# Performance work log

Hardware: AMD Instinct MI355X
Metric: run time of the kernel (lower is better)

## Reference

```python
import jax, jax.numpy as jnp
import numpy as np

N_PIX = 65536   # 256x256 render
N_GAUSS = 2048
N_COL = 3


def setup_inputs() -> dict:
    key = jax.random.key(0)
    k1, k2, k3, k4 = jax.random.split(key, 4)
    x = jax.random.uniform(k1, (N_PIX, 2), dtype=jnp.float32)           # pixel coords
    mus = jax.random.uniform(k2, (N_GAUSS, 2), dtype=jnp.float32)       # Gaussian means
    # SPD covariances: A A^T + sigma*I  (small spatial extent ~0.05)
    A = jax.random.normal(k3, (N_GAUSS, 2, 2), dtype=jnp.float32) * 0.05
    covs = jnp.einsum('mij,mkj->mik', A, A) + 0.01 * jnp.eye(2, dtype=jnp.float32)
    cols = jax.random.uniform(k4, (N_GAUSS, N_COL), dtype=jnp.float32)  # RGB per Gaussian
    return {"x": x, "mus": mus, "covs": covs, "cols": cols}


def reference(x, mus, covs, cols):
    # d: [N, M, 2] pixel-to-mean offsets
    d = x[:, None, :] - mus[None, :, :]
    # solve(covs, d) per (pixel, Gaussian) == cov_inv @ d; covs depend only on Gaussian,
    # so invert once per Gaussian (same math as torch.linalg.solve per pair).
    cov_inv = jnp.linalg.inv(covs)                      # [M, 2, 2]
    maha = jnp.einsum('nmi,mij,nmj->nm', d, cov_inv, d)  # [N, M] Mahalanobis distances
    w = jnp.exp(-0.5 * maha)                             # [N, M] Gaussian weights
    # weighted sum of colors over Gaussians: [N, M] @ [M, 3] -> [N, 3]
    return jnp.einsum('nm,mc->nc', w, cols)
```

## Files before the change

kernel.cpp:

```cpp
#include <hip/hip_runtime.h>

#define N_PIX   65536
#define N_GAUSS 2048

typedef __bf16 bf16x8 __attribute__((ext_vector_type(8)));
typedef float  f32x4  __attribute__((ext_vector_type(4)));

union BF8U { uint4 u; bf16x8 h; };
__device__ inline bf16x8 as_bf(uint4 u) { BF8U x; x.u = u; return x.h; }

__device__ inline unsigned short bfbits(float f) {
  __bf16 h = (__bf16)f;
  return __builtin_bit_cast(unsigned short, h);
}
__device__ inline float bf2f(unsigned short b) {
  return (float)__builtin_bit_cast(__bf16, b);
}
__device__ inline unsigned pkb(unsigned short a, unsigned short b) {
  return (unsigned)a | ((unsigned)b << 16);
}
__device__ inline unsigned pk2f(float a, float b) {
  return pkb(bfbits(a), bfbits(b));
}


__global__ __launch_bounds__(256) void prep_kernel(
    const float* __restrict__ mus, const float* __restrict__ covs,
    const float* __restrict__ cols, uint4* __restrict__ ws) {
  int tid = blockIdx.x * 256 + threadIdx.x;
  if (tid < 8192) {
    int lane = tid & 63;
    int tile = tid >> 6;
    int grp  = lane >> 4;
    int g    = tile * 16 + (lane & 15);
    float c00 = covs[4*g+0], c01 = covs[4*g+1];
    float c10 = covs[4*g+2], c11 = covs[4*g+3];
    float inv_det = 1.0f / (c00*c11 - c01*c10);
    float ia =  c11 * inv_det;
    float ib = -c01 * inv_det;
    float ic =  c00 * inv_det;
    float mx = mus[2*g+0], my = mus[2*g+1];
    const float kk = -0.7213475204444817f;
    float coef[6];
    coef[0] = kk * ia;
    coef[1] = kk * 2.0f * ib;
    coef[2] = kk * ic;
    coef[3] = -2.0f * kk * (ia*mx + ib*my);
    coef[4] = -2.0f * kk * (ib*mx + ic*my);
    coef[5] = kk * (ia*mx*mx + 2.0f*ib*mx*my + ic*my*my);
    unsigned short ch[6], cl[6];
    #pragma unroll
    for (int i = 0; i < 6; ++i) {
      ch[i] = bfbits(coef[i]);
      cl[i] = bfbits(coef[i] - bf2f(ch[i]));
    }
    uint4 v = make_uint4(0,0,0,0);
    if (grp == 0)      v = make_uint4(pkb(ch[0],ch[1]), pkb(ch[2],ch[3]), pkb(ch[4],ch[5]), pkb(cl[0],cl[1]));
    else if (grp == 1) v = make_uint4(pkb(cl[2],cl[3]), pkb(cl[4],cl[5]), pkb(ch[0],ch[1]), pkb(ch[2],ch[3]));
    else if (grp == 2) v = make_uint4(pkb(ch[4],ch[5]), pkb(cl[0],cl[1]), pkb(cl[2],cl[3]), pkb(cl[4],cl[5]));
    ws[tid] = v;
  } else if (tid < 12288) {
    int t2   = tid - 8192;
    int lane = t2 & 63;
    int tile = t2 >> 6;
    int rgb  = lane & 15;
    int kb   = (lane >> 4) * 8;
    uint4 v = make_uint4(0,0,0,0);
    if (rgb < 3) {
      unsigned short b[8];
      #pragma unroll
      for (int j = 0; j < 8; ++j)
        b[j] = bfbits(cols[(tile*32 + kb + j)*3 + rgb]);
      v = make_uint4(pkb(b[0],b[1]), pkb(b[2],b[3]), pkb(b[4],b[5]), pkb(b[6],b[7]));
    }
    ws[8192 + t2] = v;
  }
}

__global__ __launch_bounds__(512, 4) void render_kernel(
    const float2* __restrict__ x, const uint4* __restrict__ ws,
    float* __restrict__ out) {
  __shared__ uint4 smem[1536];
  const uint4* gq  = ws;
  const uint4* pvc = ws + 8192;

  int tid  = threadIdx.x;
  int lane = tid & 63, wave = tid >> 6;
  int c    = lane & 15, grp = lane >> 4;
  int wpix = blockIdx.x * 128 + wave * 16;

  float2 p = x[wpix + c];
  float mono[6] = {p.x*p.x, p.x*p.y, p.y*p.y, p.x, p.y, 1.0f};
  unsigned short ph[6], pl[6];
  #pragma unroll
  for (int i = 0; i < 6; ++i) {
    ph[i] = bfbits(mono[i]);
    pl[i] = bfbits(mono[i] - bf2f(ph[i]));
  }
  uint4 pv4 = make_uint4(0,0,0,0);
  if (grp == 0)      pv4 = make_uint4(pkb(ph[0],ph[1]), pkb(ph[2],ph[3]), pkb(ph[4],ph[5]), pkb(ph[0],ph[1]));
  else if (grp == 1) pv4 = make_uint4(pkb(ph[2],ph[3]), pkb(ph[4],ph[5]), pkb(pl[0],pl[1]), pkb(pl[2],pl[3]));
  else if (grp == 2) pv4 = make_uint4(pkb(pl[4],pl[5]), pkb(pl[0],pl[1]), pkb(pl[2],pl[3]), pkb(pl[4],pl[5]));
  bf16x8 pf = as_bf(pv4);

  char* Wb = (char*)smem + 16384 + (wave << 10);
  int b0 = c*64 + grp*8;
  int b1 = c*64 + 32 + grp*8;
  int br = c*64 + grp*16;
  uint2* wp0 = (uint2*)(Wb + (b0 ^ (((b0 >> 7) & 3) << 4)));
  uint2* wp1 = (uint2*)(Wb + (b1 ^ (((b1 >> 7) & 3) << 4)));
  const uint4* rp = (const uint4*)(Wb + (br ^ (((br >> 7) & 3) << 4)));

  f32x4 acc  = {0.f, 0.f, 0.f, 0.f};
  const f32x4 zero = {0.f, 0.f, 0.f, 0.f};

  uint4 s0 = gq[tid], s1 = gq[512 + tid];
  for (int chk = 0; chk < 8; ++chk) {
    __syncthreads();
    smem[tid] = s0; smem[512 + tid] = s1;
    __syncthreads();
    if (chk < 7) {
      s0 = gq[(chk+1)*1024 + tid];
      s1 = gq[(chk+1)*1024 + 512 + tid];
    }
    uint4 cf[8];
    #pragma unroll
    for (int t = 0; t < 8; ++t)
      cf[t] = pvc[chk*512 + t*64 + lane];
    #pragma unroll
    for (int pr = 0; pr < 8; ++pr) {
      uint4 ga = smem[(2*pr+0)*64 + lane];
      uint4 gb = smem[(2*pr+1)*64 + lane];
      f32x4 q0 = __builtin_amdgcn_mfma_f32_16x16x32_bf16(as_bf(ga), pf, zero, 0, 0, 0);
      f32x4 q1 = __builtin_amdgcn_mfma_f32_16x16x32_bf16(as_bf(gb), pf, zero, 0, 0, 0);
      uint2 w0, w1;
      w0.x = pk2f(__builtin_amdgcn_exp2f(q0[0]), __builtin_amdgcn_exp2f(q0[1]));
      w0.y = pk2f(__builtin_amdgcn_exp2f(q0[2]), __builtin_amdgcn_exp2f(q0[3]));
      w1.x = pk2f(__builtin_amdgcn_exp2f(q1[0]), __builtin_amdgcn_exp2f(q1[1]));
      w1.y = pk2f(__builtin_amdgcn_exp2f(q1[2]), __builtin_amdgcn_exp2f(q1[3]));
      *wp0 = w0;
      *wp1 = w1;
      asm volatile("s_waitcnt lgkmcnt(0)" ::: "memory");
      uint4 wf = *rp;
      acc = __builtin_amdgcn_mfma_f32_16x16x32_bf16(as_bf(wf), as_bf(cf[pr]), acc, 0, 0, 0);
    }
  }
  if (c < 3) {
    int pix = wpix + grp * 4;
    out[(pix+0)*3 + c] = acc[0];
    out[(pix+1)*3 + c] = acc[1];
    out[(pix+2)*3 + c] = acc[2];
    out[(pix+3)*3 + c] = acc[3];
  }
}

extern "C" void kernel_launch(void* const* d_in, const int* in_sizes, int n_in,
                              void* d_out, int out_size, void* d_ws, size_t ws_size,
                              hipStream_t stream) {
  const float* x    = (const float*)d_in[0];
  const float* mus  = (const float*)d_in[1];
  const float* covs = (const float*)d_in[2];
  const float* cols = (const float*)d_in[3];
  float* out = (float*)d_out;
  uint4* ws  = (uint4*)d_ws;

  prep_kernel<<<48, 256, 0, stream>>>(mus, covs, cols, ws);
  render_kernel<<<512, 512, 0, stream>>>((const float2*)x, ws, out);
}
```

Before: 84.87 us.

## Feed exp weights directly as MFMA operand, removing LDS transpose round-trip

Swaps the operand roles in the second MFMA so the packed exp2 results held in registers can serve directly as the B operand. The prep kernel reorders the color-tile K indices to match the register layout of the first MFMA's output. This removes a per-iteration LDS write, waitcnt and read, and shrinks shared memory. The output store now writes three channels per pixel from one lane group.

```diff
diff --git a/kernel.cpp b/kernel.cpp
--- a/kernel.cpp
+++ b/kernel.cpp
@@ -64,13 +64,15 @@
     int lane = t2 & 63;
     int tile = t2 >> 6;
     int rgb  = lane & 15;
-    int kb   = (lane >> 4) * 8;
+    int grp  = lane >> 4;
     uint4 v = make_uint4(0,0,0,0);
     if (rgb < 3) {
       unsigned short b[8];
       #pragma unroll
-      for (int j = 0; j < 8; ++j)
-        b[j] = bfbits(cols[(tile*32 + kb + j)*3 + rgb]);
+      for (int j = 0; j < 8; ++j) {
+        int sig = 4*grp + (j & 3) + ((j >> 2) ? 16 : 0);
+        b[j] = bfbits(cols[(tile*32 + sig)*3 + rgb]);
+      }
       v = make_uint4(pkb(b[0],b[1]), pkb(b[2],b[3]), pkb(b[4],b[5]), pkb(b[6],b[7]));
     }
     ws[8192 + t2] = v;
@@ -80,13 +82,14 @@
 __global__ __launch_bounds__(512, 4) void render_kernel(
     const float2* __restrict__ x, const uint4* __restrict__ ws,
     float* __restrict__ out) {
-  __shared__ uint4 smem[1536];
+  __shared__ uint4 smem[1024];
   const uint4* gq  = ws;
   const uint4* pvc = ws + 8192;
 
   int tid  = threadIdx.x;
-  int lane = tid & 63, wave = tid >> 6;
+  int lane = tid & 63;
   int c    = lane & 15, grp = lane >> 4;
+  int wave = tid >> 6;
   int wpix = blockIdx.x * 128 + wave * 16;
 
   float2 p = x[wpix + c];
@@ -102,14 +105,6 @@
   else if (grp == 1) pv4 = make_uint4(pkb(ph[2],ph[3]), pkb(ph[4],ph[5]), pkb(pl[0],pl[1]), pkb(pl[2],pl[3]));
   else if (grp == 2) pv4 = make_uint4(pkb(pl[4],pl[5]), pkb(pl[0],pl[1]), pkb(pl[2],pl[3]), pkb(pl[4],pl[5]));
   bf16x8 pf = as_bf(pv4);
-
-  char* Wb = (char*)smem + 16384 + (wave << 10);
-  int b0 = c*64 + grp*8;
-  int b1 = c*64 + 32 + grp*8;
-  int br = c*64 + grp*16;
-  uint2* wp0 = (uint2*)(Wb + (b0 ^ (((b0 >> 7) & 3) << 4)));
-  uint2* wp1 = (uint2*)(Wb + (b1 ^ (((b1 >> 7) & 3) << 4)));
-  const uint4* rp = (const uint4*)(Wb + (br ^ (((br >> 7) & 3) << 4)));
 
   f32x4 acc  = {0.f, 0.f, 0.f, 0.f};
   const f32x4 zero = {0.f, 0.f, 0.f, 0.f};
@@ -133,24 +128,19 @@
       uint4 gb = smem[(2*pr+1)*64 + lane];
       f32x4 q0 = __builtin_amdgcn_mfma_f32_16x16x32_bf16(as_bf(ga), pf, zero, 0, 0, 0);
       f32x4 q1 = __builtin_amdgcn_mfma_f32_16x16x32_bf16(as_bf(gb), pf, zero, 0, 0, 0);
-      uint2 w0, w1;
-      w0.x = pk2f(__builtin_amdgcn_exp2f(q0[0]), __builtin_amdgcn_exp2f(q0[1]));
-      w0.y = pk2f(__builtin_amdgcn_exp2f(q0[2]), __builtin_amdgcn_exp2f(q0[3]));
-      w1.x = pk2f(__builtin_amdgcn_exp2f(q1[0]), __builtin_amdgcn_exp2f(q1[1]));
-      w1.y = pk2f(__builtin_amdgcn_exp2f(q1[2]), __builtin_amdgcn_exp2f(q1[3]));
-      *wp0 = w0;
-      *wp1 = w1;
-      asm volatile("s_waitcnt lgkmcnt(0)" ::: "memory");
-      uint4 wf = *rp;
-      acc = __builtin_amdgcn_mfma_f32_16x16x32_bf16(as_bf(wf), as_bf(cf[pr]), acc, 0, 0, 0);
+      unsigned w0 = pk2f(__builtin_amdgcn_exp2f(q0[0]), __builtin_amdgcn_exp2f(q0[1]));
+      unsigned w1 = pk2f(__builtin_amdgcn_exp2f(q0[2]), __builtin_amdgcn_exp2f(q0[3]));
+      unsigned w2 = pk2f(__builtin_amdgcn_exp2f(q1[0]), __builtin_amdgcn_exp2f(q1[1]));
+      unsigned w3 = pk2f(__builtin_amdgcn_exp2f(q1[2]), __builtin_amdgcn_exp2f(q1[3]));
+      uint4 wf = make_uint4(w0, w1, w2, w3);
+      acc = __builtin_amdgcn_mfma_f32_16x16x32_bf16(as_bf(cf[pr]), as_bf(wf), acc, 0, 0, 0);
     }
   }
-  if (c < 3) {
-    int pix = wpix + grp * 4;
-    out[(pix+0)*3 + c] = acc[0];
-    out[(pix+1)*3 + c] = acc[1];
-    out[(pix+2)*3 + c] = acc[2];
-    out[(pix+3)*3 + c] = acc[3];
+  if (grp == 0) {
+    int pix = wpix + c;
+    out[pix*3 + 0] = acc[0];
+    out[pix*3 + 1] = acc[1];
+    out[pix*3 + 2] = acc[2];
   }
 }
 
```

New measurement: 82.16 us. 3.2% less time.
